# Kernel tuning notes

Hardware: AMD Instinct MI355X
Metric: run time of the kernel (lower is better)

The kernel has to match this reference:

```python
import jax, jax.numpy as jnp
import numpy as np

B, T, C, H = 8, 512, 1024, 16
N = C // H
DW, DA, DG = 64, 64, 128  # LoRA dims for decay / icl-rate / gate at C=1024

def _ln(x, w, b, eps=1e-5):
    mu = x.mean(-1, keepdims=True)
    var = ((x - mu) ** 2).mean(-1, keepdims=True)
    return (x - mu) * jax.lax.rsqrt(var + eps) * w + b

def _gn_heads(x, w, b, eps=64e-5):
    # GroupNorm(H groups) over channel dim of (B,T,C)
    xh = x.reshape(x.shape[0], x.shape[1], H, N)
    mu = xh.mean(-1, keepdims=True)
    var = ((xh - mu) ** 2).mean(-1, keepdims=True)
    xh = (xh - mu) * jax.lax.rsqrt(var + eps)
    return xh.reshape(x.shape) * w + b

def _shift(x):
    # RWKV time_shift: ZeroPad2d((0,0,1,-1))
    return jnp.concatenate([jnp.zeros_like(x[:, :1]), x[:, :-1]], axis=1)

def _wkv7(r, w_log, k, v, a, b):
    # all (B,T,H,N); state S (B,H,N,N): S = S*diag(exp(-exp(w))) + (S@a)b^T + v k^T; out = S@r
    decay = jnp.exp(-jnp.exp(w_log))
    def step(state, inp):
        r_t, d_t, k_t, v_t, a_t, b_t = inp
        sa = jnp.einsum('bhij,bhj->bhi', state, a_t)
        state = (state * d_t[:, :, None, :]
                 + sa[..., None] * b_t[:, :, None, :]
                 + v_t[..., None] * k_t[:, :, None, :])
        return state, jnp.einsum('bhij,bhj->bhi', state, r_t)
    xs = tuple(jnp.moveaxis(t, 1, 0) for t in (r, decay, k, v, a, b))
    s0 = jnp.zeros((r.shape[0], H, N, N), r.dtype)
    _, out = jax.lax.scan(step, s0, xs)
    return jnp.moveaxis(out, 0, 1)

def reference(x, v_first, ln_pre_w, ln_pre_b, ln_attn_w, ln_attn_b, ln_ffn_w, ln_ffn_b,
              x_r, x_w, x_k, x_v, x_a, x_g, w0, w1, w2, a0, a1, a2, g1, g2,
              k_k, k_a, r_k, W_r, W_k, W_v, W_o, gn_w, gn_b,
              ffn_x_k, W_ffn1, W_ffn2):
    Bx, Tx = x.shape[0], x.shape[1]
    x = _ln(x, ln_pre_w, ln_pre_b)            # pre_norm (layer_idx==0)
    # --- time mixing (RWKV7Attention) ---
    xn = _ln(x, ln_attn_w, ln_attn_b)
    dx = _shift(xn) - xn
    xr = xn + dx * x_r; xw = xn + dx * x_w; xk = xn + dx * x_k
    xv = xn + dx * x_v; xa = xn + dx * x_a; xg = xn + dx * x_g
    r = xr @ W_r
    w_log = -jax.nn.softplus(-(w0 + jnp.tanh(xw @ w1) @ w2)) - 0.5
    k = xk @ W_k
    v = xv @ W_v
    v_first = v                               # layer 0 stores v
    a = jax.nn.sigmoid(a0 + (xa @ a1) @ a2)   # in-context learning rate
    g = jax.nn.sigmoid(xg @ g1) @ g2          # gate
    kk = (k * k_k).reshape(Bx, Tx, H, N)
    kk = kk / jnp.maximum(jnp.linalg.norm(kk, axis=-1, keepdims=True), 1e-12)
    k = k * (1.0 + (a - 1.0) * k_a)
    rh = r.reshape(Bx, Tx, H, N)
    kh = k.reshape(Bx, Tx, H, N)
    vh = v.reshape(Bx, Tx, H, N)
    ah = a.reshape(Bx, Tx, H, N)
    o = _wkv7(rh, w_log.reshape(Bx, Tx, H, N), kh, vh, -kk, kk * ah)
    o = _gn_heads(o.reshape(Bx, Tx, C), gn_w, gn_b)
    o = o + ((rh * kh * r_k).sum(-1, keepdims=True) * vh).reshape(Bx, Tx, C)
    x = x + (o * g) @ W_o                     # residual (dropout p=0)
    # --- channel mixing (RWKV7FeedForward) ---
    xf = _ln(x, ln_ffn_w, ln_ffn_b)
    kf = xf + (_shift(xf) - xf) * ffn_x_k
    x = x + jnp.square(jax.nn.relu(kf @ W_ffn1)) @ W_ffn2
    return x, v_first

def setup_inputs() -> dict:
    key = jax.random.key(0)
    ks = iter(jax.random.split(key, 40))
    def nrm(shape, s=0.02):
        return jax.random.normal(next(ks), shape, jnp.float32) * s
    f32 = jnp.float32
    d = {
        'x': jax.random.normal(next(ks), (B, T, C), f32),
        'v_first': jnp.zeros((B, T, C), f32),
        'ln_pre_w': jnp.ones((C,), f32), 'ln_pre_b': jnp.zeros((C,), f32),
        'ln_attn_w': jnp.ones((C,), f32), 'ln_attn_b': jnp.zeros((C,), f32),
        'ln_ffn_w': jnp.ones((C,), f32), 'ln_ffn_b': jnp.zeros((C,), f32),
        'x_r': nrm((C,), 0.1), 'x_w': nrm((C,), 0.1), 'x_k': nrm((C,), 0.1),
        'x_v': nrm((C,), 0.1), 'x_a': nrm((C,), 0.1), 'x_g': nrm((C,), 0.1),
        'w0': nrm((C,), 0.5), 'w1': nrm((C, DW)), 'w2': nrm((DW, C)),
        'a0': nrm((C,), 0.1), 'a1': nrm((C, DA)), 'a2': nrm((DA, C)),
        'g1': nrm((C, DG)), 'g2': nrm((DG, C)),
        'k_k': 0.85 * jnp.ones((C,), f32) + nrm((C,), 0.05),
        'k_a': jnp.ones((C,), f32),
        'r_k': nrm((H, N), 0.1),
        'W_r': nrm((C, C)), 'W_k': nrm((C, C)), 'W_v': nrm((C, C)), 'W_o': nrm((C, C)),
        'gn_w': jnp.ones((C,), f32), 'gn_b': jnp.zeros((C,), f32),
        'ffn_x_k': nrm((C,), 0.1),
        'W_ffn1': nrm((C, 4 * C)), 'W_ffn2': nrm((4 * C, C)),
    }
    return d
```

## Files before the change

### kernel.cpp

```cpp
#include <hip/hip_runtime.h>

#define Bb 8
#define Tt 512
#define Cc 1024
#define Hh 16
#define Nh 64
#define Mm 4096
#define BTC 4194304
#define DEV __device__ __forceinline__

typedef __attribute__((ext_vector_type(8))) short short8;
typedef __attribute__((ext_vector_type(4))) float f32x4;

DEV unsigned short f2bf(float f) {
  unsigned int u = __builtin_bit_cast(unsigned int, f);
  u += 0x7fffu + ((u >> 16) & 1u);
  return (unsigned short)(u >> 16);
}

DEV float bflo(unsigned int u) { return __builtin_bit_cast(float, u << 16); }
DEV float bfhi(unsigned int u) { return __builtin_bit_cast(float, u & 0xFFFF0000u); }

template <int CTRL>
DEV float dppadd(float x) {
  int xi = __builtin_bit_cast(int, x);
  int yi = __builtin_amdgcn_update_dpp(0, xi, CTRL, 0xF, 0xF, true);
  return x + __builtin_bit_cast(float, yi);
}

struct TDesc { const float* in; unsigned short* out; int K, N, bstart, nbx; };
struct TPack { TDesc d[12]; };

__global__ __launch_bounds__(256) void kt_transpose_multi(TPack p) {
  __shared__ float tile[32][33];
  const int bid = blockIdx.x;
  int i = 0;
  #pragma unroll
  for (int j = 1; j < 12; ++j) if (bid >= p.d[j].bstart) i = j;
  const float* in = p.d[i].in;
  unsigned short* out = p.d[i].out;
  const int K = p.d[i].K, N = p.d[i].N;
  const int local = bid - p.d[i].bstart;
  const int byq = local / p.d[i].nbx;
  const int bx = (local - byq * p.d[i].nbx) * 32;
  const int by = byq * 32;
  int tx = threadIdx.x, ty = threadIdx.y;
  #pragma unroll
  for (int q = ty; q < 32; q += 8) {
    int kk = by + q, nn = bx + tx;
    tile[q][tx] = (kk < K && nn < N) ? in[(size_t)kk * N + nn] : 0.f;
  }
  __syncthreads();
  #pragma unroll
  for (int q = ty; q < 32; q += 8) {
    int nn = bx + q, kk = by + tx;
    if (nn < N && kk < K) out[(size_t)nn * K + kk] = f2bf(tile[tx][q]);
  }
}

DEV void row_stats(float v0, float v1, float v2, float v3, float* red,
                   float& mu, float& rs, float eps) {
  float s = v0 + v1 + v2 + v3;
  float q = v0 * v0 + v1 * v1 + v2 * v2 + v3 * v3;
  #pragma unroll
  for (int o = 32; o; o >>= 1) { s += __shfl_down(s, o); q += __shfl_down(q, o); }
  int w = threadIdx.x >> 6;
  __syncthreads();
  if ((threadIdx.x & 63) == 0) { red[w] = s; red[4 + w] = q; }
  __syncthreads();
  s = red[0] + red[1] + red[2] + red[3];
  q = red[4] + red[5] + red[6] + red[7];
  mu = s * (1.f / 1024.f);
  float var = q * (1.f / 1024.f) - mu * mu;
  rs = rsqrtf(var + eps);
}

__global__ __launch_bounds__(256) void k1_mix(
    const float* __restrict__ x,
    const float* __restrict__ lnpw, const float* __restrict__ lnpb,
    const float* __restrict__ lnaw, const float* __restrict__ lnab,
    const float* __restrict__ cr, const float* __restrict__ cw,
    const float* __restrict__ ck, const float* __restrict__ cv,
    const float* __restrict__ ca, const float* __restrict__ cg,
    float* __restrict__ xln,
    unsigned short* __restrict__ mR, unsigned short* __restrict__ mW,
    unsigned short* __restrict__ mK, unsigned short* __restrict__ mV,
    unsigned short* __restrict__ mA, unsigned short* __restrict__ mG) {
  __shared__ float red[8];
  const int row = blockIdx.x;
  const int t = row & (Tt - 1);
  const int tid = threadIdx.x;
  const int c = tid * 4;
  const size_t base = (size_t)row * Cc + c;
  float a0 = x[base], a1 = x[base + 1], a2 = x[base + 2], a3 = x[base + 3];
  float mu, rs;
  row_stats(a0, a1, a2, a3, red, mu, rs, 1e-5f);
  float pw0 = lnpw[c], pw1 = lnpw[c + 1], pw2 = lnpw[c + 2], pw3 = lnpw[c + 3];
  float pb0 = lnpb[c], pb1 = lnpb[c + 1], pb2 = lnpb[c + 2], pb3 = lnpb[c + 3];
  float l0 = (a0 - mu) * rs * pw0 + pb0, l1 = (a1 - mu) * rs * pw1 + pb1;
  float l2 = (a2 - mu) * rs * pw2 + pb2, l3 = (a3 - mu) * rs * pw3 + pb3;
  float4 st; st.x = l0; st.y = l1; st.z = l2; st.w = l3;
  *(float4*)(xln + base) = st;
  row_stats(l0, l1, l2, l3, red, mu, rs, 1e-5f);
  float aw0 = lnaw[c], aw1 = lnaw[c + 1], aw2 = lnaw[c + 2], aw3 = lnaw[c + 3];
  float ab0 = lnab[c], ab1 = lnab[c + 1], ab2 = lnab[c + 2], ab3 = lnab[c + 3];
  float n0 = (l0 - mu) * rs * aw0 + ab0, n1 = (l1 - mu) * rs * aw1 + ab1;
  float n2 = (l2 - mu) * rs * aw2 + ab2, n3 = (l3 - mu) * rs * aw3 + ab3;
  float p0 = 0.f, p1 = 0.f, p2 = 0.f, p3 = 0.f;
  if (t > 0) {
    const size_t pb_ = base - Cc;
    float q0 = x[pb_], q1 = x[pb_ + 1], q2 = x[pb_ + 2], q3 = x[pb_ + 3];
    row_stats(q0, q1, q2, q3, red, mu, rs, 1e-5f);
    float e0 = (q0 - mu) * rs * pw0 + pb0, e1 = (q1 - mu) * rs * pw1 + pb1;
    float e2 = (q2 - mu) * rs * pw2 + pb2, e3 = (q3 - mu) * rs * pw3 + pb3;
    row_stats(e0, e1, e2, e3, red, mu, rs, 1e-5f);
    p0 = (e0 - mu) * rs * aw0 + ab0; p1 = (e1 - mu) * rs * aw1 + ab1;
    p2 = (e2 - mu) * rs * aw2 + ab2; p3 = (e3 - mu) * rs * aw3 + ab3;
  }
  float d0 = p0 - n0, d1 = p1 - n1, d2 = p2 - n2, d3 = p3 - n3;
  #define EMIT(cf, dst) { \
    float f0 = cf[c], f1 = cf[c + 1], f2 = cf[c + 2], f3 = cf[c + 3]; \
    ushort4 u; u.x = f2bf(n0 + d0 * f0); u.y = f2bf(n1 + d1 * f1); \
    u.z = f2bf(n2 + d2 * f2); u.w = f2bf(n3 + d3 * f3); \
    *(ushort4*)(dst + base) = u; }
  EMIT(cr, mR) EMIT(cw, mW) EMIT(ck, mK) EMIT(cv, mV) EMIT(ca, mA) EMIT(cg, mG)
  #undef EMIT
}

DEV void gll16(const unsigned short* g, unsigned short* l) {
  __builtin_amdgcn_global_load_lds(
      (const __attribute__((address_space(1))) void*)g,
      (__attribute__((address_space(3))) void*)l, 16, 0, 0);
}

template <int MODE>
DEV void gemm_epi(float z, size_t oi, int col,
                  float* outF, unsigned short* outB,
                  const float* bias, const float* res) {
  if constexpr (MODE == 0) outF[oi] = z;
  else if constexpr (MODE == 1) outB[oi] = f2bf(z);
  else if constexpr (MODE == 2) outB[oi] = f2bf(tanhf(z));
  else if constexpr (MODE == 3) outB[oi] = f2bf(1.f / (1.f + expf(-z)));
  else if constexpr (MODE == 4) { float m = fmaxf(z, 0.f); outB[oi] = f2bf(m * m); }
  else if constexpr (MODE == 5) { z += bias[col]; outF[oi] = 1.f / (1.f + expf(-z)); }
  else if constexpr (MODE == 6) {
    z += bias[col];
    float sg = 1.f / (1.f + expf(-z));
    outF[oi] = expf(-0.6065306597126334f * sg);
  } else { outF[oi] = z + res[oi]; }
}

template <int MODE>
DEV void gemm_body(const unsigned short* A, const unsigned short* Bt,
                   int Nn, int K,
                   float* outF, unsigned short* outB,
                   const float* bias, const float* res,
                   unsigned short* lsA, unsigned short* lsB,
                   int m0, int n0) {
  const int tid = threadIdx.x;
  const int lane = tid & 63;
  const int wave = tid >> 6;
  const int wy = wave >> 1, wx = wave & 1;
  const int sl4 = lane >> 2;
  const int sc = (lane & 3) << 3;
  f32x4 acc[4][2];
  #pragma unroll
  for (int i = 0; i < 4; ++i)
    #pragma unroll
    for (int j = 0; j < 2; ++j) { f32x4 z = {0.f, 0.f, 0.f, 0.f}; acc[i][j] = z; }
  const int fr = lane & 15;
  const int fk = (lane >> 4) << 3;
  for (int k0 = 0; k0 < K; k0 += 32) {
    #pragma unroll
    for (int j = 0; j < 2; ++j) {
      const int rb = (wave + j * 4) * 16;
      gll16(A + (size_t)(m0 + rb + sl4) * K + k0 + sc, lsA + rb * 32);
    }
    {
      const int rb = wave * 16;
      int br = n0 + rb + sl4;
      br = br < Nn ? br : Nn - 1;
      gll16(Bt + (size_t)br * K + k0 + sc, lsB + rb * 32);
    }
    __syncthreads();
    short8 af[4], bf[2];
    #pragma unroll
    for (int mt = 0; mt < 4; ++mt)
      af[mt] = *(const short8*)(lsA + (wy * 64 + mt * 16 + fr) * 32 + fk);
    #pragma unroll
    for (int nt = 0; nt < 2; ++nt)
      bf[nt] = *(const short8*)(lsB + (wx * 32 + nt * 16 + fr) * 32 + fk);
    #pragma unroll
    for (int mt = 0; mt < 4; ++mt)
      #pragma unroll
      for (int nt = 0; nt < 2; ++nt)
        acc[mt][nt] = __builtin_amdgcn_mfma_f32_16x16x32_bf16(af[mt], bf[nt], acc[mt][nt], 0, 0, 0);
    __syncthreads();
  }
  const int rbase = (lane >> 4) << 2;
  const int cbase = lane & 15;
  #pragma unroll
  for (int mt = 0; mt < 4; ++mt)
    #pragma unroll
    for (int nt = 0; nt < 2; ++nt)
      #pragma unroll
      for (int rr = 0; rr < 4; ++rr) {
        int row = m0 + wy * 64 + mt * 16 + rbase + rr;
        int col = n0 + wx * 32 + nt * 16 + cbase;
        if (col < Nn)
          gemm_epi<MODE>(acc[mt][nt][rr], (size_t)row * Nn + col, col, outF, outB, bias, res);
      }
}

template <int MODE>
__global__ __launch_bounds__(256) void kg_gemm(
    const unsigned short* __restrict__ A, const unsigned short* __restrict__ Bt,
    int M, int Nn, int K,
    float* __restrict__ outF, unsigned short* __restrict__ outB,
    const float* __restrict__ bias, const float* __restrict__ res) {
  __shared__ unsigned short lsA[128 * 32];
  __shared__ unsigned short lsB[64 * 32];
  gemm_body<MODE>(A, Bt, Nn, K, outF, outB, bias, res, lsA, lsB,
                  blockIdx.y * 128, blockIdx.x * 64);
}

__global__ __launch_bounds__(256) void kg_gemm_qkv(
    const unsigned short* __restrict__ A0, const unsigned short* __restrict__ A1,
    const unsigned short* __restrict__ A2,
    const unsigned short* __restrict__ B0, const unsigned short* __restrict__ B1,
    const unsigned short* __restrict__ B2,
    float* __restrict__ O0, float* __restrict__ O1, float* __restrict__ O2) {
  __shared__ unsigned short lsA[128 * 32];
  __shared__ unsigned short lsB[64 * 32];
  const int z = blockIdx.z;
  const unsigned short* A = z == 0 ? A0 : z == 1 ? A1 : A2;
  const unsigned short* Bt = z == 0 ? B0 : z == 1 ? B1 : B2;
  float* outF = z == 0 ? O0 : z == 1 ? O1 : O2;
  gemm_body<0>(A, Bt, 1024, 1024, outF, nullptr, nullptr, nullptr, lsA, lsB,
               blockIdx.y * 128, blockIdx.x * 64);
}

template <int MODE>
__global__ __launch_bounds__(256) void kg_gemm2(
    const unsigned short* __restrict__ A, const unsigned short* __restrict__ Bt,
    int M, int Nn, int K,
    float* __restrict__ outF, unsigned short* __restrict__ outB,
    const float* __restrict__ bias, const float* __restrict__ res) {
  __shared__ unsigned short lsA[128 * 32];
  __shared__ unsigned short lsB[128 * 32];
  const int tid = threadIdx.x;
  const int lane = tid & 63;
  const int wave = tid >> 6;
  const int wy = wave >> 1, wx = wave & 1;
  const int m0 = blockIdx.y * 128;
  const int n0 = blockIdx.x * 128;
  const int sl4 = lane >> 2;
  const int sc = (lane & 3) << 3;
  f32x4 acc[4][4];
  #pragma unroll
  for (int i = 0; i < 4; ++i)
    #pragma unroll
    for (int j = 0; j < 4; ++j) { f32x4 z = {0.f, 0.f, 0.f, 0.f}; acc[i][j] = z; }
  const int fr = lane & 15;
  const int fk = (lane >> 4) << 3;
  for (int k0 = 0; k0 < K; k0 += 32) {
    #pragma unroll
    for (int j = 0; j < 2; ++j) {
      const int rb = (wave + j * 4) * 16;
      gll16(A + (size_t)(m0 + rb + sl4) * K + k0 + sc, lsA + rb * 32);
      int br = n0 + rb + sl4;
      br = br < Nn ? br : Nn - 1;
      gll16(Bt + (size_t)br * K + k0 + sc, lsB + rb * 32);
    }
    __syncthreads();
    short8 af[4], bf[4];
    #pragma unroll
    for (int mt = 0; mt < 4; ++mt)
      af[mt] = *(const short8*)(lsA + (wy * 64 + mt * 16 + fr) * 32 + fk);
    #pragma unroll
    for (int nt = 0; nt < 4; ++nt)
      bf[nt] = *(const short8*)(lsB + (wx * 64 + nt * 16 + fr) * 32 + fk);
    #pragma unroll
    for (int mt = 0; mt < 4; ++mt)
      #pragma unroll
      for (int nt = 0; nt < 4; ++nt)
        acc[mt][nt] = __builtin_amdgcn_mfma_f32_16x16x32_bf16(af[mt], bf[nt], acc[mt][nt], 0, 0, 0);
    __syncthreads();
  }
  const int rbase = (lane >> 4) << 2;
  const int cbase = lane & 15;
  #pragma unroll
  for (int mt = 0; mt < 4; ++mt)
    #pragma unroll
    for (int nt = 0; nt < 4; ++nt)
      #pragma unroll
      for (int rr = 0; rr < 4; ++rr) {
        int row = m0 + wy * 64 + mt * 16 + rbase + rr;
        int col = n0 + wx * 64 + nt * 16 + cbase;
        if (col < Nn)
          gemm_epi<MODE>(acc[mt][nt][rr], (size_t)row * Nn + col, col, outF, outB, bias, res);
      }
}

__global__ __launch_bounds__(256) void k4_prep(
    float* __restrict__ k, const float* __restrict__ a,
    const float* __restrict__ kkc, const float* __restrict__ kac,
    unsigned short* __restrict__ awh, unsigned short* __restrict__ bwh,
    unsigned short* __restrict__ kh) {
  const int row = blockIdx.x, tid = threadIdx.x;
  const int c = tid * 4;
  const size_t base = (size_t)row * Cc + c;
  float k0 = k[base], k1 = k[base + 1], k2 = k[base + 2], k3 = k[base + 3];
  float a0 = a[base], a1 = a[base + 1], a2 = a[base + 2], a3 = a[base + 3];
  float h0 = k0 * kkc[c], h1 = k1 * kkc[c + 1], h2 = k2 * kkc[c + 2], h3 = k3 * kkc[c + 3];
  float ss = h0 * h0 + h1 * h1 + h2 * h2 + h3 * h3;
  #pragma unroll
  for (int m = 8; m; m >>= 1) ss += __shfl_xor(ss, m);
  float inv = 1.f / fmaxf(sqrtf(ss), 1e-12f);
  h0 *= inv; h1 *= inv; h2 *= inv; h3 *= inv;
  ushort4 u;
  u.x = f2bf(-h0); u.y = f2bf(-h1); u.z = f2bf(-h2); u.w = f2bf(-h3);
  *(ushort4*)(awh + base) = u;
  u.x = f2bf(h0 * a0); u.y = f2bf(h1 * a1); u.z = f2bf(h2 * a2); u.w = f2bf(h3 * a3);
  *(ushort4*)(bwh + base) = u;
  float n0 = k0 * (1.f + (a0 - 1.f) * kac[c]);
  float n1 = k1 * (1.f + (a1 - 1.f) * kac[c + 1]);
  float n2 = k2 * (1.f + (a2 - 1.f) * kac[c + 2]);
  float n3 = k3 * (1.f + (a3 - 1.f) * kac[c + 3]);
  u.x = f2bf(n0); u.y = f2bf(n1); u.z = f2bf(n2); u.w = f2bf(n3);
  *(ushort4*)(kh + base) = u;
  float4 v4; v4.x = n0; v4.y = n1; v4.z = n2; v4.w = n3;
  *(float4*)(k + base) = v4;
}

#define CS 8
__global__ __launch_bounds__(512, 2) void k5_wkv7(
    const float* __restrict__ r, const float* __restrict__ dec,
    const float* __restrict__ v,
    const unsigned short* __restrict__ awh, const unsigned short* __restrict__ bwh,
    const unsigned short* __restrict__ kh,
    float* __restrict__ o) {
  const int blk = blockIdx.x;
  const int bh = blk & 127, half = blk >> 7;
  const int b = bh >> 4, h = bh & 15;
  const int tid = threadIdx.x;
  const int lane = tid & 63;
  const int w = tid >> 6;
  const int cg = lane & 15;
  const int rw = lane >> 4;
  const int row = half * 32 + w * 4 + rw;
  const int cb = cg << 2;

  __shared__ float buf[2][2304];

  float S[4];
  #pragma unroll
  for (int j = 0; j < 4; ++j) S[j] = 0.f;

  const size_t base = (size_t)b * Tt * Cc + (size_t)h * Nh;

  const int srow = lane >> 4, scol = (lane & 15) << 2;
  const int hrow = lane >> 3, hcol = (lane & 7) << 3;

  uint4 R0, R1;
  #define LOADC(cstart) { \
    if (w < 3) { \
      const float* sp = w == 0 ? dec : w == 1 ? v : r; \
      const size_t g0 = base + (size_t)((cstart) + srow) * Cc + scol; \
      R0 = *(const uint4*)(sp + g0); \
      R1 = *(const uint4*)(sp + g0 + 4 * Cc); \
    } else if (w < 6) { \
      const unsigned short* sp = w == 3 ? awh : w == 4 ? bwh : kh; \
      const size_t g0 = base + (size_t)((cstart) + hrow) * Cc + hcol; \
      R0 = *(const uint4*)(sp + g0); \
    } }

  LOADC(0)

  #pragma unroll 1
  for (int c = 0; c < Tt / CS; ++c) {
    float* bp = buf[c & 1];
    if (w < 3) {
      *(uint4*)(bp + w * 512 + (lane << 2)) = R0;
      *(uint4*)(bp + w * 512 + 256 + (lane << 2)) = R1;
    } else if (w < 6) {
      unsigned short* hb = (unsigned short*)(bp + 1536);
      *(uint4*)(hb + (w - 3) * 512 + lane * 8) = R0;
    }
    const int cn = (c + 1 < Tt / CS) ? (c + 1) : c;
    LOADC(cn * CS)
    __syncthreads();

    float4 Dq[2], Rq[2];
    uint2 Ah[2], Bh[2], Kh[2];
    float Vv[2];
    #define LOADOPS(slot, ss) { \
      const float* sp_ = bp + (ss) * 64; \
      Dq[slot] = *(const float4*)(sp_ + cb); \
      Vv[slot] = sp_[512 + row]; \
      Rq[slot] = *(const float4*)(sp_ + 1024 + cb); \
      const unsigned short* hb_ = (const unsigned short*)(bp + 1536) + (ss) * 64 + cb; \
      Ah[slot] = *(const uint2*)(hb_); \
      Bh[slot] = *(const uint2*)(hb_ + 512); \
      Kh[slot] = *(const uint2*)(hb_ + 1024); }

    LOADOPS(0, 0)
    #pragma unroll
    for (int s = 0; s < CS; ++s) {
      const int cu = s & 1, nx = cu ^ 1;
      if (s + 1 < CS) LOADOPS(nx, s + 1)

      float ax = bflo(Ah[cu].x), ay = bfhi(Ah[cu].x);
      float az = bflo(Ah[cu].y), aw_ = bfhi(Ah[cu].y);
      float sa = fmaf(S[1], ay, S[0] * ax) + fmaf(S[3], aw_, S[2] * az);
      sa = dppadd<0xB1>(sa);
      sa = dppadd<0x4E>(sa);
      sa = dppadd<0x124>(sa);
      sa = dppadd<0x128>(sa);

      float bx = bflo(Bh[cu].x), by = bfhi(Bh[cu].x);
      float bz = bflo(Bh[cu].y), bw_ = bfhi(Bh[cu].y);
      float kx = bflo(Kh[cu].x), ky = bfhi(Kh[cu].x);
      float kz = bflo(Kh[cu].y), kw_ = bfhi(Kh[cu].y);
      const float vv = Vv[cu];
      float4 d4 = Dq[cu], r4 = Rq[cu];
      S[0] = fmaf(S[0], d4.x, fmaf(vv, kx, sa * bx));
      float oo = S[0] * r4.x;
      S[1] = fmaf(S[1], d4.y, fmaf(vv, ky, sa * by));
      oo = fmaf(S[1], r4.y, oo);
      S[2] = fmaf(S[2], d4.z, fmaf(vv, kz, sa * bz));
      oo = fmaf(S[2], r4.z, oo);
      S[3] = fmaf(S[3], d4.w, fmaf(vv, kw_, sa * bw_));
      oo = fmaf(S[3], r4.w, oo);

      oo = dppadd<0xB1>(oo);
      oo = dppadd<0x4E>(oo);
      oo = dppadd<0x124>(oo);
      oo = dppadd<0x128>(oo);
      if (cg == 0) o[base + (size_t)(c * CS + s) * Cc + row] = oo;
    }
    #undef LOADOPS
  }
  #undef LOADC
}

__global__ __launch_bounds__(256) void k6_out(
    const float* __restrict__ o, const float* __restrict__ r, const float* __restrict__ k,
    const float* __restrict__ v, const float* __restrict__ rk,
    const float* __restrict__ gnw, const float* __restrict__ gnb,
    const float* __restrict__ g, unsigned short* __restrict__ og) {
  const int row = blockIdx.x, tid = threadIdx.x;
  const int c = tid * 4;
  const size_t base = (size_t)row * Cc + c;
  float o0 = o[base], o1 = o[base + 1], o2 = o[base + 2], o3 = o[base + 3];
  float r0 = r[base], r1 = r[base + 1], r2 = r[base + 2], r3 = r[base + 3];
  float k0 = k[base], k1 = k[base + 1], k2 = k[base + 2], k3 = k[base + 3];
  float s = o0 + o1 + o2 + o3;
  float q = o0 * o0 + o1 * o1 + o2 * o2 + o3 * o3;
  float bs = r0 * k0 * rk[c] + r1 * k1 * rk[c + 1] + r2 * k2 * rk[c + 2] + r3 * k3 * rk[c + 3];
  #pragma unroll
  for (int m = 8; m; m >>= 1) {
    s += __shfl_xor(s, m); q += __shfl_xor(q, m); bs += __shfl_xor(bs, m);
  }
  float mu = s * (1.f / 64.f);
  float var = q * (1.f / 64.f) - mu * mu;
  float rs = rsqrtf(var + 64e-5f);
  float v0 = v[base], v1 = v[base + 1], v2 = v[base + 2], v3 = v[base + 3];
  float z0 = (o0 - mu) * rs * gnw[c] + gnb[c] + bs * v0;
  float z1 = (o1 - mu) * rs * gnw[c + 1] + gnb[c + 1] + bs * v1;
  float z2 = (o2 - mu) * rs * gnw[c + 2] + gnb[c + 2] + bs * v2;
  float z3 = (o3 - mu) * rs * gnw[c + 3] + gnb[c + 3] + bs * v3;
  ushort4 u;
  u.x = f2bf(z0 * g[base]); u.y = f2bf(z1 * g[base + 1]);
  u.z = f2bf(z2 * g[base + 2]); u.w = f2bf(z3 * g[base + 3]);
  *(ushort4*)(og + base) = u;
}

__global__ __launch_bounds__(256) void k8_ffnmix(
    const float* __restrict__ x2, const float* __restrict__ lnw, const float* __restrict__ lnb,
    const float* __restrict__ fxk, unsigned short* __restrict__ kf) {
  __shared__ float red[8];
  const int row = blockIdx.x;
  const int t = row & (Tt - 1);
  const int tid = threadIdx.x;
  const int c = tid * 4;
  const size_t base = (size_t)row * Cc + c;
  float a0 = x2[base], a1 = x2[base + 1], a2 = x2[base + 2], a3 = x2[base + 3];
  float mu, rs;
  row_stats(a0, a1, a2, a3, red, mu, rs, 1e-5f);
  float w0 = lnw[c], w1 = lnw[c + 1], w2 = lnw[c + 2], w3 = lnw[c + 3];
  float b0 = lnb[c], b1 = lnb[c + 1], b2 = lnb[c + 2], b3 = lnb[c + 3];
  float f0 = (a0 - mu) * rs * w0 + b0, f1 = (a1 - mu) * rs * w1 + b1;
  float f2 = (a2 - mu) * rs * w2 + b2, f3 = (a3 - mu) * rs * w3 + b3;
  float p0 = 0.f, p1 = 0.f, p2 = 0.f, p3 = 0.f;
  if (t > 0) {
    const size_t pb_ = base - Cc;
    float q0 = x2[pb_], q1 = x2[pb_ + 1], q2 = x2[pb_ + 2], q3 = x2[pb_ + 3];
    row_stats(q0, q1, q2, q3, red, mu, rs, 1e-5f);
    p0 = (q0 - mu) * rs * w0 + b0; p1 = (q1 - mu) * rs * w1 + b1;
    p2 = (q2 - mu) * rs * w2 + b2; p3 = (q3 - mu) * rs * w3 + b3;
  }
  ushort4 u;
  u.x = f2bf(f0 + (p0 - f0) * fxk[c]);
  u.y = f2bf(f1 + (p1 - f1) * fxk[c + 1]);
  u.z = f2bf(f2 + (p2 - f2) * fxk[c + 2]);
  u.w = f2bf(f3 + (p3 - f3) * fxk[c + 3]);
  *(ushort4*)(kf + base) = u;
}

extern "C" void kernel_launch(void* const* d_in, const int* in_sizes, int n_in,
                              void* d_out, int out_size, void* d_ws, size_t ws_size,
                              hipStream_t stream) {
  (void)in_sizes; (void)n_in; (void)out_size; (void)ws_size;
  const float* x    = (const float*)d_in[0];
  const float* lnpw = (const float*)d_in[2];
  const float* lnpb = (const float*)d_in[3];
  const float* lnaw = (const float*)d_in[4];
  const float* lnab = (const float*)d_in[5];
  const float* lnfw = (const float*)d_in[6];
  const float* lnfb = (const float*)d_in[7];
  const float* cxr  = (const float*)d_in[8];
  const float* cxw  = (const float*)d_in[9];
  const float* cxk  = (const float*)d_in[10];
  const float* cxv  = (const float*)d_in[11];
  const float* cxa  = (const float*)d_in[12];
  const float* cxg  = (const float*)d_in[13];
  const float* w0v  = (const float*)d_in[14];
  const float* w1m  = (const float*)d_in[15];
  const float* w2m  = (const float*)d_in[16];
  const float* a0v  = (const float*)d_in[17];
  const float* a1m  = (const float*)d_in[18];
  const float* a2m  = (const float*)d_in[19];
  const float* g1m  = (const float*)d_in[20];
  const float* g2m  = (const float*)d_in[21];
  const float* kkv  = (const float*)d_in[22];
  const float* kav  = (const float*)d_in[23];
  const float* rkv  = (const float*)d_in[24];
  const float* Wr   = (const float*)d_in[25];
  const float* Wk   = (const float*)d_in[26];
  const float* Wv   = (const float*)d_in[27];
  const float* Wo   = (const float*)d_in[28];
  const float* gnw  = (const float*)d_in[29];
  const float* gnb  = (const float*)d_in[30];
  const float* fxk  = (const float*)d_in[31];
  const float* Wf1  = (const float*)d_in[32];
  const float* Wf2  = (const float*)d_in[33];

  char* ws = (char*)d_ws;
  float* outx = (float*)d_out;
  float* vout = outx + BTC;

  size_t off = 0;
  unsigned short* WrT  = (unsigned short*)(ws + off); off += 2097152;
  unsigned short* WkT  = (unsigned short*)(ws + off); off += 2097152;
  unsigned short* WvT  = (unsigned short*)(ws + off); off += 2097152;
  unsigned short* WoT  = (unsigned short*)(ws + off); off += 2097152;
  unsigned short* Wf1T = (unsigned short*)(ws + off); off += 8388608;
  unsigned short* Wf2T = (unsigned short*)(ws + off); off += 8388608;
  unsigned short* w1T  = (unsigned short*)(ws + off); off += 131072;
  unsigned short* w2T  = (unsigned short*)(ws + off); off += 131072;
  unsigned short* a1T  = (unsigned short*)(ws + off); off += 131072;
  unsigned short* a2T  = (unsigned short*)(ws + off); off += 131072;
  unsigned short* g1T  = (unsigned short*)(ws + off); off += 262144;
  unsigned short* g2T  = (unsigned short*)(ws + off); off += 262144;
  float* xln = (float*)(ws + off); off += 16777216;
  unsigned short* mixR = (unsigned short*)(ws + off);
  unsigned short* mixW = (unsigned short*)(ws + off + 8388608);
  unsigned short* mixK = (unsigned short*)(ws + off + 16777216);
  unsigned short* mixV = (unsigned short*)(ws + off + 25165824);
  unsigned short* mixA = (unsigned short*)(ws + off + 33554432);
  unsigned short* mixG = (unsigned short*)(ws + off + 41943040);
  unsigned short* hbuf = (unsigned short*)(ws + off);
  off += 50331648;
  unsigned short* tmpw = (unsigned short*)(ws + off); off += 524288;
  unsigned short* tmpa = (unsigned short*)(ws + off); off += 524288;
  unsigned short* tmpg = (unsigned short*)(ws + off); off += 1048576;
  float* decay = (float*)(ws + off);
  unsigned short* og = (unsigned short*)(ws + off);
  off += 16777216;
  float* aicl = (float*)(ws + off);
  float* obuf = (float*)(ws + off);
  off += 16777216;
  float* gout = (float*)(ws + off); off += 16777216;
  float* rbuf = (float*)(ws + off);
  float* x2   = (float*)(ws + off);
  off += 16777216;
  float* kbuf = (float*)(ws + off); off += 16777216;
  unsigned short* awh = (unsigned short*)(ws + off);
  unsigned short* kf  = (unsigned short*)(ws + off);
  unsigned short* bwh = awh + BTC;
  off += 16777216;
  unsigned short* khb = (unsigned short*)(ws + off);
  off += 16777216;

  dim3 tb(32, 8);
  TPack tp;
  tp.d[0]  = TDesc{Wr,  WrT,  1024, 1024, 0,     32};
  tp.d[1]  = TDesc{Wk,  WkT,  1024, 1024, 1024,  32};
  tp.d[2]  = TDesc{Wv,  WvT,  1024, 1024, 2048,  32};
  tp.d[3]  = TDesc{Wo,  WoT,  1024, 1024, 3072,  32};
  tp.d[4]  = TDesc{Wf1, Wf1T, 1024, 4096, 4096,  128};
  tp.d[5]  = TDesc{Wf2, Wf2T, 4096, 1024, 8192,  32};
  tp.d[6]  = TDesc{w1m, w1T,  1024, 64,   12288, 2};
  tp.d[7]  = TDesc{w2m, w2T,  64,   1024, 12352, 32};
  tp.d[8]  = TDesc{a1m, a1T,  1024, 64,   12416, 2};
  tp.d[9]  = TDesc{a2m, a2T,  64,   1024, 12480, 32};
  tp.d[10] = TDesc{g1m, g1T,  1024, 128,  12544, 4};
  tp.d[11] = TDesc{g2m, g2T,  128,  1024, 12672, 32};
  kt_transpose_multi<<<12800, tb, 0, stream>>>(tp);

  k1_mix<<<Mm, 256, 0, stream>>>(x, lnpw, lnpb, lnaw, lnab, cxr, cxw, cxk, cxv, cxa, cxg,
                                 xln, mixR, mixW, mixK, mixV, mixA, mixG);

  kg_gemm<2><<<dim3(1, 32), 256, 0, stream>>>(mixW, w1T, Mm, 64, 1024, nullptr, tmpw, nullptr, nullptr);
  kg_gemm<6><<<dim3(16, 32), 256, 0, stream>>>(tmpw, w2T, Mm, 1024, 64, decay, nullptr, w0v, nullptr);
  kg_gemm<1><<<dim3(1, 32), 256, 0, stream>>>(mixA, a1T, Mm, 64, 1024, nullptr, tmpa, nullptr, nullptr);
  kg_gemm<5><<<dim3(16, 32), 256, 0, stream>>>(tmpa, a2T, Mm, 1024, 64, aicl, nullptr, a0v, nullptr);
  kg_gemm<3><<<dim3(2, 32), 256, 0, stream>>>(mixG, g1T, Mm, 128, 1024, nullptr, tmpg, nullptr, nullptr);
  kg_gemm<0><<<dim3(16, 32), 256, 0, stream>>>(tmpg, g2T, Mm, 1024, 128, gout, nullptr, nullptr, nullptr);

  kg_gemm_qkv<<<dim3(16, 32, 3), 256, 0, stream>>>(mixR, mixK, mixV, WrT, WkT, WvT,
                                                   rbuf, kbuf, vout);

  k4_prep<<<Mm, 256, 0, stream>>>(kbuf, aicl, kkv, kav, awh, bwh, khb);
  k5_wkv7<<<256, 512, 0, stream>>>(rbuf, decay, vout, awh, bwh, khb, obuf);
  k6_out<<<Mm, 256, 0, stream>>>(obuf, rbuf, kbuf, vout, rkv, gnw, gnb, gout, og);
  kg_gemm<7><<<dim3(16, 32), 256, 0, stream>>>(og, WoT, Mm, 1024, 1024, x2, nullptr, nullptr, xln);
  k8_ffnmix<<<Mm, 256, 0, stream>>>(x2, lnfw, lnfb, fxk, kf);
  kg_gemm2<4><<<dim3(32, 32), 256, 0, stream>>>(kf, Wf1T, Mm, 4096, 1024, nullptr, hbuf, nullptr, nullptr);
  kg_gemm<7><<<dim3(16, 32), 256, 0, stream>>>(hbuf, Wf2T, Mm, 1024, 4096, outx, nullptr, nullptr, x2);
}
```

Measured before the change: 636.5 us.

## Batch LoRA GEMMs, widen big GEMM tiles, switch WKV operands to fp32

```diff
diff --git a/kernel.cpp b/kernel.cpp
--- a/kernel.cpp
+++ b/kernel.cpp
@@ -17,9 +17,6 @@
   u += 0x7fffu + ((u >> 16) & 1u);
   return (unsigned short)(u >> 16);
 }
-
-DEV float bflo(unsigned int u) { return __builtin_bit_cast(float, u << 16); }
-DEV float bfhi(unsigned int u) { return __builtin_bit_cast(float, u & 0xFFFF0000u); }
 
 template <int CTRL>
 DEV float dppadd(float x) {
@@ -150,13 +147,22 @@
   } else { outF[oi] = z + res[oi]; }
 }
 
-template <int MODE>
-DEV void gemm_body(const unsigned short* A, const unsigned short* Bt,
-                   int Nn, int K,
-                   float* outF, unsigned short* outB,
-                   const float* bias, const float* res,
-                   unsigned short* lsA, unsigned short* lsB,
-                   int m0, int n0) {
+DEV void gemm_epi_rt(int mode, float z, size_t oi, int col,
+                     float* outF, unsigned short* outB, const float* bias) {
+  if (mode == 0) outF[oi] = z;
+  else if (mode == 1) outB[oi] = f2bf(z);
+  else if (mode == 2) outB[oi] = f2bf(tanhf(z));
+  else if (mode == 3) outB[oi] = f2bf(1.f / (1.f + expf(-z)));
+  else if (mode == 5) { z += bias[col]; outF[oi] = 1.f / (1.f + expf(-z)); }
+  else { z += bias[col]; float sg = 1.f / (1.f + expf(-z));
+         outF[oi] = expf(-0.6065306597126334f * sg); }
+}
+
+DEV void gemm_body_rt(const unsigned short* A, const unsigned short* Bt,
+                      int Nn, int K,
+                      float* outF, unsigned short* outB, const float* bias,
+                      unsigned short* lsA, unsigned short* lsB,
+                      int m0, int n0, int mode) {
   const int tid = threadIdx.x;
   const int lane = tid & 63;
   const int wave = tid >> 6;
@@ -208,52 +214,61 @@
         int row = m0 + wy * 64 + mt * 16 + rbase + rr;
         int col = n0 + wx * 32 + nt * 16 + cbase;
         if (col < Nn)
-          gemm_epi<MODE>(acc[mt][nt][rr], (size_t)row * Nn + col, col, outF, outB, bias, res);
+          gemm_epi_rt(mode, acc[mt][nt][rr], (size_t)row * Nn + col, col, outF, outB, bias);
       }
 }
 
-template <int MODE>
-__global__ __launch_bounds__(256) void kg_gemm(
-    const unsigned short* __restrict__ A, const unsigned short* __restrict__ Bt,
-    int M, int Nn, int K,
-    float* __restrict__ outF, unsigned short* __restrict__ outB,
-    const float* __restrict__ bias, const float* __restrict__ res) {
-  __shared__ unsigned short lsA[128 * 32];
-  __shared__ unsigned short lsB[64 * 32];
-  gemm_body<MODE>(A, Bt, Nn, K, outF, outB, bias, res, lsA, lsB,
-                  blockIdx.y * 128, blockIdx.x * 64);
-}
-
-__global__ __launch_bounds__(256) void kg_gemm_qkv(
-    const unsigned short* __restrict__ A0, const unsigned short* __restrict__ A1,
-    const unsigned short* __restrict__ A2,
-    const unsigned short* __restrict__ B0, const unsigned short* __restrict__ B1,
-    const unsigned short* __restrict__ B2,
-    float* __restrict__ O0, float* __restrict__ O1, float* __restrict__ O2) {
+__global__ __launch_bounds__(256) void kg_lora1(
+    const unsigned short* __restrict__ mW, const unsigned short* __restrict__ mA,
+    const unsigned short* __restrict__ mG,
+    const unsigned short* __restrict__ w1T, const unsigned short* __restrict__ a1T,
+    const unsigned short* __restrict__ g1T,
+    unsigned short* __restrict__ tmpw, unsigned short* __restrict__ tmpa,
+    unsigned short* __restrict__ tmpg) {
   __shared__ unsigned short lsA[128 * 32];
   __shared__ unsigned short lsB[64 * 32];
   const int z = blockIdx.z;
-  const unsigned short* A = z == 0 ? A0 : z == 1 ? A1 : A2;
-  const unsigned short* Bt = z == 0 ? B0 : z == 1 ? B1 : B2;
-  float* outF = z == 0 ? O0 : z == 1 ? O1 : O2;
-  gemm_body<0>(A, Bt, 1024, 1024, outF, nullptr, nullptr, nullptr, lsA, lsB,
-               blockIdx.y * 128, blockIdx.x * 64);
+  const unsigned short* A  = z == 0 ? mW : z == 1 ? mA : mG;
+  const unsigned short* Bt = z == 0 ? w1T : z == 1 ? a1T : g1T;
+  unsigned short* outB     = z == 0 ? tmpw : z == 1 ? tmpa : tmpg;
+  const int Nn = z < 2 ? 64 : 128;
+  const int n0 = z < 2 ? 0 : (z - 2) * 64;
+  const int mode = z == 0 ? 2 : z == 1 ? 1 : 3;
+  gemm_body_rt(A, Bt, Nn, 1024, nullptr, outB, nullptr, lsA, lsB,
+               blockIdx.y * 128, n0, mode);
+}
+
+__global__ __launch_bounds__(256) void kg_lora2(
+    const unsigned short* __restrict__ tmpw, const unsigned short* __restrict__ tmpa,
+    const unsigned short* __restrict__ tmpg,
+    const unsigned short* __restrict__ w2T, const unsigned short* __restrict__ a2T,
+    const unsigned short* __restrict__ g2T,
+    float* __restrict__ decay, float* __restrict__ aicl, float* __restrict__ gout,
+    const float* __restrict__ w0v, const float* __restrict__ a0v) {
+  __shared__ unsigned short lsA[128 * 32];
+  __shared__ unsigned short lsB[64 * 32];
+  const int z = blockIdx.z;
+  const unsigned short* A  = z == 0 ? tmpw : z == 1 ? tmpa : tmpg;
+  const unsigned short* Bt = z == 0 ? w2T : z == 1 ? a2T : g2T;
+  float* outF              = z == 0 ? decay : z == 1 ? aicl : gout;
+  const float* bias        = z == 0 ? w0v : z == 1 ? a0v : nullptr;
+  const int K = z < 2 ? 64 : 128;
+  const int mode = z == 0 ? 6 : z == 1 ? 5 : 0;
+  gemm_body_rt(A, Bt, 1024, K, outF, nullptr, bias, lsA, lsB,
+               blockIdx.y * 128, blockIdx.x * 64, mode);
 }
 
 template <int MODE>
-__global__ __launch_bounds__(256) void kg_gemm2(
-    const unsigned short* __restrict__ A, const unsigned short* __restrict__ Bt,
-    int M, int Nn, int K,
-    float* __restrict__ outF, unsigned short* __restrict__ outB,
-    const float* __restrict__ bias, const float* __restrict__ res) {
-  __shared__ unsigned short lsA[128 * 32];
-  __shared__ unsigned short lsB[128 * 32];
+DEV void gemm2_body(const unsigned short* A, const unsigned short* Bt,
+                    int Nn, int K,
+                    float* outF, unsigned short* outB,
+                    const float* bias, const float* res,
+                    unsigned short* lsA, unsigned short* lsB,
+                    int m0, int n0) {
   const int tid = threadIdx.x;
   const int lane = tid & 63;
   const int wave = tid >> 6;
   const int wy = wave >> 1, wx = wave & 1;
-  const int m0 = blockIdx.y * 128;
-  const int n0 = blockIdx.x * 128;
   const int sl4 = lane >> 2;
   const int sc = (lane & 3) << 3;
   f32x4 acc[4][4];
@@ -302,11 +317,38 @@
       }
 }
 
+template <int MODE>
+__global__ __launch_bounds__(256) void kg_gemm2(
+    const unsigned short* __restrict__ A, const unsigned short* __restrict__ Bt,
+    int M, int Nn, int K,
+    float* __restrict__ outF, unsigned short* __restrict__ outB,
+    const float* __restrict__ bias, const float* __restrict__ res) {
+  __shared__ unsigned short lsA[128 * 32];
+  __shared__ unsigned short lsB[128 * 32];
+  gemm2_body<MODE>(A, Bt, Nn, K, outF, outB, bias, res, lsA, lsB,
+                   blockIdx.y * 128, blockIdx.x * 128);
+}
+
+__global__ __launch_bounds__(256) void kg_gemm2_qkv(
+    const unsigned short* __restrict__ A0, const unsigned short* __restrict__ A1,
+    const unsigned short* __restrict__ A2,
+    const unsigned short* __restrict__ B0, const unsigned short* __restrict__ B1,
+    const unsigned short* __restrict__ B2,
+    float* __restrict__ O0, float* __restrict__ O1, float* __restrict__ O2) {
+  __shared__ unsigned short lsA[128 * 32];
+  __shared__ unsigned short lsB[128 * 32];
+  const int z = blockIdx.z;
+  const unsigned short* A = z == 0 ? A0 : z == 1 ? A1 : A2;
+  const unsigned short* Bt = z == 0 ? B0 : z == 1 ? B1 : B2;
+  float* outF = z == 0 ? O0 : z == 1 ? O1 : O2;
+  gemm2_body<0>(A, Bt, 1024, 1024, outF, nullptr, nullptr, nullptr, lsA, lsB,
+                blockIdx.y * 128, blockIdx.x * 128);
+}
+
 __global__ __launch_bounds__(256) void k4_prep(
     float* __restrict__ k, const float* __restrict__ a,
     const float* __restrict__ kkc, const float* __restrict__ kac,
-    unsigned short* __restrict__ awh, unsigned short* __restrict__ bwh,
-    unsigned short* __restrict__ kh) {
+    float* __restrict__ aw, float* __restrict__ bw) {
   const int row = blockIdx.x, tid = threadIdx.x;
   const int c = tid * 4;
   const size_t base = (size_t)row * Cc + c;
@@ -318,27 +360,23 @@
   for (int m = 8; m; m >>= 1) ss += __shfl_xor(ss, m);
   float inv = 1.f / fmaxf(sqrtf(ss), 1e-12f);
   h0 *= inv; h1 *= inv; h2 *= inv; h3 *= inv;
-  ushort4 u;
-  u.x = f2bf(-h0); u.y = f2bf(-h1); u.z = f2bf(-h2); u.w = f2bf(-h3);
-  *(ushort4*)(awh + base) = u;
-  u.x = f2bf(h0 * a0); u.y = f2bf(h1 * a1); u.z = f2bf(h2 * a2); u.w = f2bf(h3 * a3);
-  *(ushort4*)(bwh + base) = u;
-  float n0 = k0 * (1.f + (a0 - 1.f) * kac[c]);
-  float n1 = k1 * (1.f + (a1 - 1.f) * kac[c + 1]);
-  float n2 = k2 * (1.f + (a2 - 1.f) * kac[c + 2]);
-  float n3 = k3 * (1.f + (a3 - 1.f) * kac[c + 3]);
-  u.x = f2bf(n0); u.y = f2bf(n1); u.z = f2bf(n2); u.w = f2bf(n3);
-  *(ushort4*)(kh + base) = u;
-  float4 v4; v4.x = n0; v4.y = n1; v4.z = n2; v4.w = n3;
+  float4 v4;
+  v4.x = -h0; v4.y = -h1; v4.z = -h2; v4.w = -h3;
+  *(float4*)(aw + base) = v4;
+  v4.x = h0 * a0; v4.y = h1 * a1; v4.z = h2 * a2; v4.w = h3 * a3;
+  *(float4*)(bw + base) = v4;
+  v4.x = k0 * (1.f + (a0 - 1.f) * kac[c]);
+  v4.y = k1 * (1.f + (a1 - 1.f) * kac[c + 1]);
+  v4.z = k2 * (1.f + (a2 - 1.f) * kac[c + 2]);
+  v4.w = k3 * (1.f + (a3 - 1.f) * kac[c + 3]);
   *(float4*)(k + base) = v4;
 }
 
 #define CS 8
 __global__ __launch_bounds__(512, 2) void k5_wkv7(
     const float* __restrict__ r, const float* __restrict__ dec,
-    const float* __restrict__ v,
-    const unsigned short* __restrict__ awh, const unsigned short* __restrict__ bwh,
-    const unsigned short* __restrict__ kh,
+    const float* __restrict__ k, const float* __restrict__ v,
+    const float* __restrict__ aw, const float* __restrict__ bw,
     float* __restrict__ o) {
   const int blk = blockIdx.x;
   const int bh = blk & 127, half = blk >> 7;
@@ -351,7 +389,7 @@
   const int row = half * 32 + w * 4 + rw;
   const int cb = cg << 2;
 
-  __shared__ float buf[2][2304];
+  __shared__ float buf[2][6 * CS * 64];
 
   float S[4];
   #pragma unroll
@@ -359,50 +397,40 @@
 
   const size_t base = (size_t)b * Tt * Cc + (size_t)h * Nh;
 
-  const int srow = lane >> 4, scol = (lane & 15) << 2;
-  const int hrow = lane >> 3, hcol = (lane & 7) << 3;
+  const float* sptr = w == 0 ? aw : w == 1 ? dec : w == 2 ? bw
+                    : w == 3 ? k  : w == 4 ? r   : v;
+  const int srow = lane >> 4;
+  const int scol = (lane & 15) << 2;
 
   uint4 R0, R1;
-  #define LOADC(cstart) { \
-    if (w < 3) { \
-      const float* sp = w == 0 ? dec : w == 1 ? v : r; \
-      const size_t g0 = base + (size_t)((cstart) + srow) * Cc + scol; \
-      R0 = *(const uint4*)(sp + g0); \
-      R1 = *(const uint4*)(sp + g0 + 4 * Cc); \
-    } else if (w < 6) { \
-      const unsigned short* sp = w == 3 ? awh : w == 4 ? bwh : kh; \
-      const size_t g0 = base + (size_t)((cstart) + hrow) * Cc + hcol; \
-      R0 = *(const uint4*)(sp + g0); \
-    } }
+  #define LOADC(cstart) if (w < 6) { \
+    const size_t g0 = base + (size_t)((cstart) + srow) * Cc + scol; \
+    R0 = *(const uint4*)(sptr + g0); \
+    R1 = *(const uint4*)(sptr + g0 + 4 * Cc); }
 
   LOADC(0)
 
   #pragma unroll 1
   for (int c = 0; c < Tt / CS; ++c) {
     float* bp = buf[c & 1];
-    if (w < 3) {
+    if (w < 6) {
       *(uint4*)(bp + w * 512 + (lane << 2)) = R0;
       *(uint4*)(bp + w * 512 + 256 + (lane << 2)) = R1;
-    } else if (w < 6) {
-      unsigned short* hb = (unsigned short*)(bp + 1536);
-      *(uint4*)(hb + (w - 3) * 512 + lane * 8) = R0;
     }
     const int cn = (c + 1 < Tt / CS) ? (c + 1) : c;
     LOADC(cn * CS)
     __syncthreads();
 
-    float4 Dq[2], Rq[2];
-    uint2 Ah[2], Bh[2], Kh[2];
+    float4 Aq[2], Dq[2], Bq[2], Kq[2], Rq[2];
     float Vv[2];
     #define LOADOPS(slot, ss) { \
       const float* sp_ = bp + (ss) * 64; \
-      Dq[slot] = *(const float4*)(sp_ + cb); \
-      Vv[slot] = sp_[512 + row]; \
-      Rq[slot] = *(const float4*)(sp_ + 1024 + cb); \
-      const unsigned short* hb_ = (const unsigned short*)(bp + 1536) + (ss) * 64 + cb; \
-      Ah[slot] = *(const uint2*)(hb_); \
-      Bh[slot] = *(const uint2*)(hb_ + 512); \
-      Kh[slot] = *(const uint2*)(hb_ + 1024); }
+      Aq[slot] = *(const float4*)(sp_ + cb); \
+      Dq[slot] = *(const float4*)(sp_ + 512 + cb); \
+      Bq[slot] = *(const float4*)(sp_ + 1024 + cb); \
+      Kq[slot] = *(const float4*)(sp_ + 1536 + cb); \
+      Rq[slot] = *(const float4*)(sp_ + 2048 + cb); \
+      Vv[slot] = sp_[2560 + row]; }
 
     LOADOPS(0, 0)
     #pragma unroll
@@ -410,27 +438,22 @@
       const int cu = s & 1, nx = cu ^ 1;
       if (s + 1 < CS) LOADOPS(nx, s + 1)
 
-      float ax = bflo(Ah[cu].x), ay = bfhi(Ah[cu].x);
-      float az = bflo(Ah[cu].y), aw_ = bfhi(Ah[cu].y);
-      float sa = fmaf(S[1], ay, S[0] * ax) + fmaf(S[3], aw_, S[2] * az);
+      float4 a4 = Aq[cu];
+      float sa = fmaf(S[1], a4.y, S[0] * a4.x) + fmaf(S[3], a4.w, S[2] * a4.z);
       sa = dppadd<0xB1>(sa);
       sa = dppadd<0x4E>(sa);
       sa = dppadd<0x124>(sa);
       sa = dppadd<0x128>(sa);
 
-      float bx = bflo(Bh[cu].x), by = bfhi(Bh[cu].x);
-      float bz = bflo(Bh[cu].y), bw_ = bfhi(Bh[cu].y);
-      float kx = bflo(Kh[cu].x), ky = bfhi(Kh[cu].x);
-      float kz = bflo(Kh[cu].y), kw_ = bfhi(Kh[cu].y);
       const float vv = Vv[cu];
-      float4 d4 = Dq[cu], r4 = Rq[cu];
-      S[0] = fmaf(S[0], d4.x, fmaf(vv, kx, sa * bx));
+      float4 d4 = Dq[cu], b4 = Bq[cu], k4 = Kq[cu], r4 = Rq[cu];
+      S[0] = fmaf(S[0], d4.x, fmaf(vv, k4.x, sa * b4.x));
       float oo = S[0] * r4.x;
-      S[1] = fmaf(S[1], d4.y, fmaf(vv, ky, sa * by));
+      S[1] = fmaf(S[1], d4.y, fmaf(vv, k4.y, sa * b4.y));
       oo = fmaf(S[1], r4.y, oo);
-      S[2] = fmaf(S[2], d4.z, fmaf(vv, kz, sa * bz));
+      S[2] = fmaf(S[2], d4.z, fmaf(vv, k4.z, sa * b4.z));
       oo = fmaf(S[2], r4.z, oo);
-      S[3] = fmaf(S[3], d4.w, fmaf(vv, kw_, sa * bw_));
+      S[3] = fmaf(S[3], d4.w, fmaf(vv, k4.w, sa * b4.w));
       oo = fmaf(S[3], r4.w, oo);
 
       oo = dppadd<0xB1>(oo);
@@ -586,12 +609,10 @@
   float* x2   = (float*)(ws + off);
   off += 16777216;
   float* kbuf = (float*)(ws + off); off += 16777216;
-  unsigned short* awh = (unsigned short*)(ws + off);
-  unsigned short* kf  = (unsigned short*)(ws + off);
-  unsigned short* bwh = awh + BTC;
+  float* awb  = (float*)(ws + off);
+  unsigned short* kf = (unsigned short*)(ws + off);
   off += 16777216;
-  unsigned short* khb = (unsigned short*)(ws + off);
-  off += 16777216;
+  float* bwb  = (float*)(ws + off); off += 16777216;
 
   dim3 tb(32, 8);
   TPack tp;
@@ -612,21 +633,19 @@
   k1_mix<<<Mm, 256, 0, stream>>>(x, lnpw, lnpb, lnaw, lnab, cxr, cxw, cxk, cxv, cxa, cxg,
                                  xln, mixR, mixW, mixK, mixV, mixA, mixG);
 
-  kg_gemm<2><<<dim3(1, 32), 256, 0, stream>>>(mixW, w1T, Mm, 64, 1024, nullptr, tmpw, nullptr, nullptr);
-  kg_gemm<6><<<dim3(16, 32), 256, 0, stream>>>(tmpw, w2T, Mm, 1024, 64, decay, nullptr, w0v, nullptr);
-  kg_gemm<1><<<dim3(1, 32), 256, 0, stream>>>(mixA, a1T, Mm, 64, 1024, nullptr, tmpa, nullptr, nullptr);
-  kg_gemm<5><<<dim3(16, 32), 256, 0, stream>>>(tmpa, a2T, Mm, 1024, 64, aicl, nullptr, a0v, nullptr);
-  kg_gemm<3><<<dim3(2, 32), 256, 0, stream>>>(mixG, g1T, Mm, 128, 1024, nullptr, tmpg, nullptr, nullptr);
-  kg_gemm<0><<<dim3(16, 32), 256, 0, stream>>>(tmpg, g2T, Mm, 1024, 128, gout, nullptr, nullptr, nullptr);
-
-  kg_gemm_qkv<<<dim3(16, 32, 3), 256, 0, stream>>>(mixR, mixK, mixV, WrT, WkT, WvT,
+  kg_lora1<<<dim3(1, 32, 4), 256, 0, stream>>>(mixW, mixA, mixG, w1T, a1T, g1T,
+                                               tmpw, tmpa, tmpg);
+  kg_lora2<<<dim3(16, 32, 3), 256, 0, stream>>>(tmpw, tmpa, tmpg, w2T, a2T, g2T,
+                                                decay, aicl, gout, w0v, a0v);
+
+  kg_gemm2_qkv<<<dim3(8, 32, 3), 256, 0, stream>>>(mixR, mixK, mixV, WrT, WkT, WvT,
                                                    rbuf, kbuf, vout);
 
-  k4_prep<<<Mm, 256, 0, stream>>>(kbuf, aicl, kkv, kav, awh, bwh, khb);
-  k5_wkv7<<<256, 512, 0, stream>>>(rbuf, decay, vout, awh, bwh, khb, obuf);
+  k4_prep<<<Mm, 256, 0, stream>>>(kbuf, aicl, kkv, kav, awb, bwb);
+  k5_wkv7<<<256, 512, 0, stream>>>(rbuf, decay, kbuf, vout, awb, bwb, obuf);
   k6_out<<<Mm, 256, 0, stream>>>(obuf, rbuf, kbuf, vout, rkv, gnw, gnb, gout, og);
-  kg_gemm<7><<<dim3(16, 32), 256, 0, stream>>>(og, WoT, Mm, 1024, 1024, x2, nullptr, nullptr, xln);
+  kg_gemm2<7><<<dim3(8, 32), 256, 0, stream>>>(og, WoT, Mm, 1024, 1024, x2, nullptr, nullptr, xln);
   k8_ffnmix<<<Mm, 256, 0, stream>>>(x2, lnfw, lnfb, fxk, kf);
   kg_gemm2<4><<<dim3(32, 32), 256, 0, stream>>>(kf, Wf1T, Mm, 4096, 1024, nullptr, hbuf, nullptr, nullptr);
-  kg_gemm<7><<<dim3(16, 32), 256, 0, stream>>>(hbuf, Wf2T, Mm, 1024, 4096, outx, nullptr, nullptr, x2);
-}
+  kg_gemm2<7><<<dim3(8, 32), 256, 0, stream>>>(hbuf, Wf2T, Mm, 1024, 4096, outx, nullptr, nullptr, x2);
+}
```

Result: faster. 619.3 us (-2.7%).
